# Optimization experiments

Measured on AMD Instinct MI355X. Metric: run time of the kernel, lower is better.

The kernel has to match this reference:

```python
import jax, jax.numpy as jnp
import numpy as np

BINS = 64

def _histc_rows(flat, bins):
    # flat: [N, L]; per-row torch.histc semantics with min=max=0 (use data min/max)
    lo = flat.min(axis=1, keepdims=True)
    hi = flat.max(axis=1, keepdims=True)
    same = hi == lo
    lo = jnp.where(same, lo - 1.0, lo)
    hi = jnp.where(same, hi + 1.0, hi)
    # bin index; value == hi maps to bins -> clipped into last bin (torch includes max)
    idx = jnp.floor((flat - lo) / (hi - lo) * bins).astype(jnp.int32)
    idx = jnp.clip(idx, 0, bins - 1)
    n = flat.shape[0]
    flat_idx = idx + (jnp.arange(n, dtype=jnp.int32)[:, None] * bins)
    hist = jnp.zeros((n * bins,), dtype=flat.dtype).at[flat_idx.ravel()].add(1.0)
    return hist.reshape(n, bins)

def reference(x, conv_w, conv_b, head_w, head_b):
    # Conv2d(1 -> C, k=3, valid), NCHW
    y = jax.lax.conv_general_dilated(
        x, conv_w, window_strides=(1, 1), padding='VALID',
        dimension_numbers=('NCHW', 'OIHW', 'NCHW'))
    y = y + conv_b[None, :, None, None]
    y = jax.nn.relu(y)
    b, c, h, w = y.shape
    hist = _histc_rows(y.reshape(b * c, h * w), BINS)  # [B*C, bins]
    feat = hist.reshape(b, c * BINS)
    return feat @ head_w.T + head_b

def setup_inputs() -> dict:
    key = jax.random.key(0)
    k1, k2, k3, k4, k5 = jax.random.split(key, 5)
    C, K, F = 64, 3, 1000
    return {
        'x': jax.random.normal(k1, (64, 1, 256, 256), dtype=jnp.float32),
        'conv_w': jax.random.normal(k2, (C, 1, K, K), dtype=jnp.float32) * 0.1,
        'conv_b': jax.random.normal(k3, (C,), dtype=jnp.float32) * 0.1,
        'head_w': jax.random.normal(k4, (F, C * BINS), dtype=jnp.float32) * 0.02,
        'head_b': jax.random.normal(k5, (F,), dtype=jnp.float32) * 0.02,
    }
```

## Files before the change

kernel.cpp:

```cpp
#include <hip/hip_runtime.h>


typedef short bf16x8 __attribute__((ext_vector_type(8)));
typedef float f32x16 __attribute__((ext_vector_type(16)));
typedef float f32x2 __attribute__((ext_vector_type(2)));

#define TPITCH 35
#define F_OUT_ 1000
#define KDIM_ 4096

__device__ __forceinline__ unsigned f2bf(float f) {
    unsigned u = __float_as_uint(f);
    return (u + 0x7FFFu + ((u >> 16) & 1u)) >> 16;
}
__device__ __forceinline__ float bf2f(unsigned h) { return __uint_as_float(h << 16); }

__device__ __forceinline__ unsigned cvt_u32_sat(float f) {
    unsigned r;
    asm volatile("v_cvt_u32_f32 %0, %1" : "=v"(r) : "v"(f));
    return r;
}

union FragU { uint4 u; bf16x8 v; };

__global__ __launch_bounds__(512, 6) void conv_minmax_kernel(
    const float* __restrict__ x, const float* __restrict__ cw,
    const float* __restrict__ cb, float* __restrict__ featQ,
    float* __restrict__ mnbuf, float* __restrict__ mxbuf)
{
    __shared__ unsigned t32[256 * TPITCH];
    __shared__ float red[1024];

    const int tid = threadIdx.x;
    const int lane = tid & 63;
    const int w = __builtin_amdgcn_readfirstlane(tid >> 6);
    const int b = blockIdx.x;
    const int seg = blockIdx.y;
    const int mrow = lane & 31;
    const int kg = lane >> 5;
    const int r0 = seg * 32;
    const int vlim = min(32, 254 - r0);

    featQ[(seg * 64 + b) * 512 + tid] = 0.f;

    FragU bwh[2], bwl[2];
#pragma unroll
    for (int g = 0; g < 2; ++g) {
        int och = g * 32 + mrow;
        unsigned hh[8], ll[8];
#pragma unroll
        for (int j = 0; j < 8; ++j) {
            int k = kg * 8 + j, dr = k >> 2, dc = k & 3;
            float wv = (kg == 1 && j == 7) ? cb[och]
                     : ((dr < 3 && dc < 3) ? cw[och * 9 + dr * 3 + dc] : 0.f);
            unsigned h = f2bf(wv);
            hh[j] = h;
            ll[j] = f2bf(wv - bf2f(h));
        }
        bwh[g].u = make_uint4(hh[0] | (hh[1] << 16), hh[2] | (hh[3] << 16),
                              hh[4] | (hh[5] << 16), hh[6] | (hh[7] << 16));
        bwl[g].u = make_uint4(ll[0] | (ll[1] << 16), ll[2] | (ll[3] << 16),
                              ll[4] | (ll[5] << 16), ll[6] | (ll[7] << 16));
    }
    f32x16 zc;
#pragma unroll
    for (int r = 0; r < 16; ++r) zc[r] = 0.f;

    const float* xb = x + (size_t)b * 65536;
    for (int i = tid; i < TPITCH * 256; i += 512) {
        int lrow = i >> 8, col = i & 255;
        int grow = r0 + lrow;
        float v = (grow < 256) ? xb[grow * 256 + col] : 0.f;
        unsigned h = f2bf(v);
        unsigned l = f2bf(v - bf2f(h));
        t32[col * TPITCH + lrow] = (l << 16) | h;
    }
    __syncthreads();

    f32x2 mn2A = {3.4e38f, 3.4e38f}, mx2A = {-3.4e38f, -3.4e38f};
    f32x2 mn2B = {3.4e38f, 3.4e38f}, mx2B = {-3.4e38f, -3.4e38f};
    const int cbase = w * 32;
    const int cend = min(cbase + 32, 254);
    const unsigned* tb = t32 + mrow + 2 * kg;
    unsigned a0 = tb[cbase * TPITCH],       r1a = tb[cbase * TPITCH + 1];
    unsigned a1 = tb[(cbase + 1) * TPITCH], r1b = tb[(cbase + 1) * TPITCH + 1];
#pragma unroll 2
    for (int c = cbase; c < cend; ++c) {
        unsigned a2 = tb[(c + 2) * TPITCH];
        unsigned r1c = tb[(c + 2) * TPITCH + 1];
        FragU ah, al;
        ah.u = make_uint4(__builtin_amdgcn_perm(a1, a0, 0x05040100u), a2,
                          __builtin_amdgcn_perm(r1b, r1a, 0x05040100u),
                          (r1c & 0xFFFFu) | 0x3F800000u);
        al.u = make_uint4(__builtin_amdgcn_perm(a1, a0, 0x07060302u), a2 >> 16,
                          __builtin_amdgcn_perm(r1b, r1a, 0x07060302u), r1c >> 16);
        a0 = a1; a1 = a2; r1a = r1b; r1b = r1c;
        f32x16 accA = __builtin_amdgcn_mfma_f32_32x32x16_bf16(ah.v, bwh[0].v, zc, 0, 0, 0);
        f32x16 accB = __builtin_amdgcn_mfma_f32_32x32x16_bf16(ah.v, bwh[1].v, zc, 0, 0, 0);
        accA = __builtin_amdgcn_mfma_f32_32x32x16_bf16(al.v, bwh[0].v, accA, 0, 0, 0);
        accB = __builtin_amdgcn_mfma_f32_32x32x16_bf16(al.v, bwh[1].v, accB, 0, 0, 0);
        accA = __builtin_amdgcn_mfma_f32_32x32x16_bf16(ah.v, bwl[0].v, accA, 0, 0, 0);
        accB = __builtin_amdgcn_mfma_f32_32x32x16_bf16(ah.v, bwl[1].v, accB, 0, 0, 0);
        if (vlim >= 32) {
#pragma unroll
            for (int r = 0; r < 16; r += 2) {
                f32x2 vA = {accA[r], accA[r + 1]}, vB = {accB[r], accB[r + 1]};
                mn2A = __builtin_elementwise_min(mn2A, vA);
                mx2A = __builtin_elementwise_max(mx2A, vA);
                mn2B = __builtin_elementwise_min(mn2B, vB);
                mx2B = __builtin_elementwise_max(mx2B, vB);
            }
        } else {
#pragma unroll
            for (int r = 0; r < 16; ++r) {
                int crow = (r & 3) + 8 * (r >> 2) + 4 * kg;
                float vA = (crow < vlim) ? accA[r] : accA[0];
                float vB = (crow < vlim) ? accB[r] : accB[0];
                mn2A[0] = fminf(mn2A[0], vA); mx2A[0] = fmaxf(mx2A[0], vA);
                mn2B[0] = fminf(mn2B[0], vB); mx2B[0] = fmaxf(mx2B[0], vB);
            }
        }
    }

    float mnA = fminf(mn2A[0], mn2A[1]), mxA = fmaxf(mx2A[0], mx2A[1]);
    float mnB = fminf(mn2B[0], mn2B[1]), mxB = fmaxf(mx2B[0], mx2B[1]);
    mnA = fminf(mnA, __shfl_xor(mnA, 32, 64));
    mxA = fmaxf(mxA, __shfl_xor(mxA, 32, 64));
    mnB = fminf(mnB, __shfl_xor(mnB, 32, 64));
    mxB = fmaxf(mxB, __shfl_xor(mxB, 32, 64));
    __syncthreads();
    if (lane < 32) {
        red[w * 64 + mrow] = mnA;        red[512 + w * 64 + mrow] = mxA;
        red[w * 64 + 32 + mrow] = mnB;   red[512 + w * 64 + 32 + mrow] = mxB;
    }
    __syncthreads();
    if (tid < 64) {
        float a = red[tid], c = red[512 + tid];
#pragma unroll
        for (int i = 1; i < 8; ++i) {
            a = fminf(a, red[i * 64 + tid]);
            c = fmaxf(c, red[512 + i * 64 + tid]);
        }
        mnbuf[((b * 64 + tid) << 3) | seg] = a;
        mxbuf[((b * 64 + tid) << 3) | seg] = c;
    }
}

__global__ __launch_bounds__(512, 6) void conv_hist_kernel(
    const float* __restrict__ x, const float* __restrict__ cw,
    const float* __restrict__ cb, float* __restrict__ featQ,
    const float* __restrict__ mnbuf, const float* __restrict__ mxbuf)
{
    __shared__ unsigned t32[256 * TPITCH];
    __shared__ unsigned hist[65 * 32];

    const int tid = threadIdx.x;
    const int lane = tid & 63;
    const int w = __builtin_amdgcn_readfirstlane(tid >> 6);
    const int b = blockIdx.x;
    const int seg = blockIdx.y;
    const int gz = blockIdx.z;
    const int mrow = lane & 31;
    const int kg = lane >> 5;
    const int r0 = seg * 32;
    const int vlim = min(32, 254 - r0);
    const int och = gz * 32 + mrow;

    float rmn = 3.402823466e38f, rmx = -3.402823466e38f;
#pragma unroll
    for (int s = 0; s < 8; ++s) {
        rmn = fminf(rmn, mnbuf[((b * 64 + och) << 3) | s]);
        rmx = fmaxf(rmx, mxbuf[((b * 64 + och) << 3) | s]);
    }
    float lo = fmaxf(rmn, 0.f);
    float hi = fmaxf(rmx, 0.f);
    if (hi == lo) { lo -= 1.f; hi += 1.f; }
    const float sc = 63.984f / (hi - lo);
    const float nls = -lo * sc;
    for (int i = tid; i < 65 * 32; i += 512) hist[i] = 0u;

    FragU bwh, bwl;
    {
        unsigned hh[8], ll[8];
#pragma unroll
        for (int j = 0; j < 8; ++j) {
            int k = kg * 8 + j, dr = k >> 2, dc = k & 3;
            float wv = (kg == 1 && j == 7) ? fmaf(cb[och], sc, nls)
                     : ((dr < 3 && dc < 3) ? cw[och * 9 + dr * 3 + dc] * sc : 0.f);
            unsigned h = f2bf(wv);
            hh[j] = h;
            ll[j] = f2bf(wv - bf2f(h));
        }
        bwh.u = make_uint4(hh[0] | (hh[1] << 16), hh[2] | (hh[3] << 16),
                           hh[4] | (hh[5] << 16), hh[6] | (hh[7] << 16));
        bwl.u = make_uint4(ll[0] | (ll[1] << 16), ll[2] | (ll[3] << 16),
                           ll[4] | (ll[5] << 16), ll[6] | (ll[7] << 16));
    }
    f32x16 zc;
#pragma unroll
    for (int r = 0; r < 16; ++r) zc[r] = 0.f;

    const float* xb = x + (size_t)b * 65536;
    for (int i = tid; i < TPITCH * 256; i += 512) {
        int lrow = i >> 8, col = i & 255;
        int grow = r0 + lrow;
        float v = (grow < 256) ? xb[grow * 256 + col] : 0.f;
        unsigned h = f2bf(v);
        unsigned l = f2bf(v - bf2f(h));
        t32[col * TPITCH + lrow] = (l << 16) | h;
    }
    __syncthreads();

    const int cbase = w * 32;
    const int cend = min(cbase + 32, 254);
    unsigned* hrow = hist + mrow;
    const unsigned* tb = t32 + mrow + 2 * kg;
    unsigned a0 = tb[cbase * TPITCH],       r1a = tb[cbase * TPITCH + 1];
    unsigned a1 = tb[(cbase + 1) * TPITCH], r1b = tb[(cbase + 1) * TPITCH + 1];
#pragma unroll 2
    for (int c = cbase; c < cend; ++c) {
        unsigned a2 = tb[(c + 2) * TPITCH];
        unsigned r1c = tb[(c + 2) * TPITCH + 1];
        FragU ah, al;
        ah.u = make_uint4(__builtin_amdgcn_perm(a1, a0, 0x05040100u), a2,
                          __builtin_amdgcn_perm(r1b, r1a, 0x05040100u),
                          (r1c & 0xFFFFu) | 0x3F800000u);
        al.u = make_uint4(__builtin_amdgcn_perm(a1, a0, 0x07060302u), a2 >> 16,
                          __builtin_amdgcn_perm(r1b, r1a, 0x07060302u), r1c >> 16);
        a0 = a1; a1 = a2; r1a = r1b; r1b = r1c;
        f32x16 acc = __builtin_amdgcn_mfma_f32_32x32x16_bf16(ah.v, bwh.v, zc, 0, 0, 0);
        acc = __builtin_amdgcn_mfma_f32_32x32x16_bf16(al.v, bwh.v, acc, 0, 0, 0);
        acc = __builtin_amdgcn_mfma_f32_32x32x16_bf16(ah.v, bwl.v, acc, 0, 0, 0);
        if (vlim >= 32) {
#pragma unroll
            for (int r = 0; r < 16; ++r) {
                unsigned bin = cvt_u32_sat(acc[r]);
                atomicAdd(&hrow[bin << 5], 1u);
            }
        } else {
#pragma unroll
            for (int r = 0; r < 16; ++r) {
                int crow = (r & 3) + 8 * (r >> 2) + 4 * kg;
                unsigned bin = cvt_u32_sat(acc[r]);
                if (crow >= vlim) bin = 64u;
                atomicAdd(&hrow[bin << 5], 1u);
            }
        }
    }
    __syncthreads();

    for (int i = tid; i < 2048; i += 512) {
        int o = i >> 6, bin = i & 63;
        float cnt = (float)hist[(bin << 5) + o];
        int k = ((gz * 32 + o) << 6) | bin;
        atomicAdd(&featQ[((k >> 2) << 8) | (b << 2) | (k & 3)], cnt);
    }
}

__global__ __launch_bounds__(512) void head_kernel(
    const float* __restrict__ featQ, const float* __restrict__ hw,
    float* __restrict__ part)
{
    __shared__ float red[8][8][64];
    const int tid = threadIdx.x;
    const int m = tid & 63;
    const int kh = __builtin_amdgcn_readfirstlane(tid >> 6);
    const int n0 = blockIdx.x * 8;
    const int q = blockIdx.y;
    const int kqbase = q * 256 + kh * 32;
    const float* fb = featQ + kqbase * 256 + (m << 2);
    const float* wp[8];
#pragma unroll
    for (int c = 0; c < 8; ++c)
        wp[c] = hw + (size_t)(n0 + c) * KDIM_ + (kqbase << 2);

    float a[8] = {0.f, 0.f, 0.f, 0.f, 0.f, 0.f, 0.f, 0.f};
#pragma unroll 2
    for (int kq = 0; kq < 32; ++kq) {
        float4 f = *(const float4*)(fb + (kq << 8));
#pragma unroll
        for (int c = 0; c < 8; ++c) {
            float4 u = *(const float4*)(wp[c] + (kq << 2));
            a[c] += f.x * u.x + f.y * u.y + f.z * u.z + f.w * u.w;
        }
    }
#pragma unroll
    for (int c = 0; c < 8; ++c) red[kh][c][m] = a[c];
    __syncthreads();
    {
        int c = tid >> 6, mm = tid & 63;
        float v = 0.f;
#pragma unroll
        for (int j = 0; j < 8; ++j) v += red[j][c][mm];
        part[(size_t)q * 64000 + (n0 + c) * 64 + mm] = v;
    }
}

__global__ __launch_bounds__(256) void head_reduce_kernel(
    const float* __restrict__ part, const float* __restrict__ hb,
    float* __restrict__ out)
{
    int idx = blockIdx.x * 256 + threadIdx.x;
    int n = idx >> 6, m = idx & 63;
    float v = hb[n] + part[idx] + part[64000 + idx] +
              part[128000 + idx] + part[192000 + idx];
    out[(size_t)m * F_OUT_ + n] = v;
}

extern "C" void kernel_launch(void* const* d_in, const int* in_sizes, int n_in,
                              void* d_out, int out_size, void* d_ws, size_t ws_size,
                              hipStream_t stream) {
    const float* x      = (const float*)d_in[0];
    const float* conv_w = (const float*)d_in[1];
    const float* conv_b = (const float*)d_in[2];
    const float* head_w = (const float*)d_in[3];
    const float* head_b = (const float*)d_in[4];
    float* out   = (float*)d_out;
    float* featQ = (float*)d_ws;
    float* mnbuf = featQ + 262144;
    float* mxbuf = mnbuf + 32768;
    float* part  = mxbuf + 32768;

    dim3 g1(64, 8);
    dim3 g2(64, 8, 2);
    conv_minmax_kernel<<<g1, 512, 0, stream>>>(x, conv_w, conv_b, featQ, mnbuf, mxbuf);
    conv_hist_kernel<<<g2, 512, 0, stream>>>(x, conv_w, conv_b, featQ, mnbuf, mxbuf);
    head_kernel<<<dim3(125, 4), 512, 0, stream>>>(featQ, head_w, part);
    head_reduce_kernel<<<250, 256, 0, stream>>>(part, head_b, out);
}
```

Measured before the change: 186.3 us.

## Merge both channel groups into one histogram block and prefetch LDS rows ahead

The histogram kernel now handles all 64 output channels per block with two MFMA accumulator sets, instead of launching a second z-slice per 32 channels. This halves the redundant input staging and bf16 split conversion of the image tile, at the cost of more registers and a larger shared histogram. Both conv kernels also load the next input column one iteration early to hide LDS latency, and replace the paired vector min/max with scalar fminf/fmaxf chains. The occupancy hint drops from 6 to 4 blocks to allow the extra register pressure.

```diff
diff --git a/kernel.cpp b/kernel.cpp
--- a/kernel.cpp
+++ b/kernel.cpp
@@ -3,7 +3,6 @@
 
 typedef short bf16x8 __attribute__((ext_vector_type(8)));
 typedef float f32x16 __attribute__((ext_vector_type(16)));
-typedef float f32x2 __attribute__((ext_vector_type(2)));
 
 #define TPITCH 35
 #define F_OUT_ 1000
@@ -23,7 +22,7 @@
 
 union FragU { uint4 u; bf16x8 v; };
 
-__global__ __launch_bounds__(512, 6) void conv_minmax_kernel(
+__global__ __launch_bounds__(512, 4) void conv_minmax_kernel(
     const float* __restrict__ x, const float* __restrict__ cw,
     const float* __restrict__ cb, float* __restrict__ featQ,
     float* __restrict__ mnbuf, float* __restrict__ mxbuf)
@@ -77,24 +76,26 @@
     }
     __syncthreads();
 
-    f32x2 mn2A = {3.4e38f, 3.4e38f}, mx2A = {-3.4e38f, -3.4e38f};
-    f32x2 mn2B = {3.4e38f, 3.4e38f}, mx2B = {-3.4e38f, -3.4e38f};
+    float mnA = 3.4e38f, mxA = -3.4e38f;
+    float mnB = 3.4e38f, mxB = -3.4e38f;
     const int cbase = w * 32;
     const int cend = min(cbase + 32, 254);
     const unsigned* tb = t32 + mrow + 2 * kg;
     unsigned a0 = tb[cbase * TPITCH],       r1a = tb[cbase * TPITCH + 1];
     unsigned a1 = tb[(cbase + 1) * TPITCH], r1b = tb[(cbase + 1) * TPITCH + 1];
+    unsigned a2 = tb[(cbase + 2) * TPITCH], r1c = tb[(cbase + 2) * TPITCH + 1];
 #pragma unroll 2
     for (int c = cbase; c < cend; ++c) {
-        unsigned a2 = tb[(c + 2) * TPITCH];
-        unsigned r1c = tb[(c + 2) * TPITCH + 1];
+        int cp = min(c + 3, 255);
+        unsigned a3  = tb[cp * TPITCH];
+        unsigned r1d = tb[cp * TPITCH + 1];
         FragU ah, al;
         ah.u = make_uint4(__builtin_amdgcn_perm(a1, a0, 0x05040100u), a2,
                           __builtin_amdgcn_perm(r1b, r1a, 0x05040100u),
                           (r1c & 0xFFFFu) | 0x3F800000u);
         al.u = make_uint4(__builtin_amdgcn_perm(a1, a0, 0x07060302u), a2 >> 16,
                           __builtin_amdgcn_perm(r1b, r1a, 0x07060302u), r1c >> 16);
-        a0 = a1; a1 = a2; r1a = r1b; r1b = r1c;
+        a0 = a1; a1 = a2; a2 = a3; r1a = r1b; r1b = r1c; r1c = r1d;
         f32x16 accA = __builtin_amdgcn_mfma_f32_32x32x16_bf16(ah.v, bwh[0].v, zc, 0, 0, 0);
         f32x16 accB = __builtin_amdgcn_mfma_f32_32x32x16_bf16(ah.v, bwh[1].v, zc, 0, 0, 0);
         accA = __builtin_amdgcn_mfma_f32_32x32x16_bf16(al.v, bwh[0].v, accA, 0, 0, 0);
@@ -104,11 +105,10 @@
         if (vlim >= 32) {
 #pragma unroll
             for (int r = 0; r < 16; r += 2) {
-                f32x2 vA = {accA[r], accA[r + 1]}, vB = {accB[r], accB[r + 1]};
-                mn2A = __builtin_elementwise_min(mn2A, vA);
-                mx2A = __builtin_elementwise_max(mx2A, vA);
-                mn2B = __builtin_elementwise_min(mn2B, vB);
-                mx2B = __builtin_elementwise_max(mx2B, vB);
+                mnA = fminf(fminf(mnA, accA[r]), accA[r + 1]);
+                mxA = fmaxf(fmaxf(mxA, accA[r]), accA[r + 1]);
+                mnB = fminf(fminf(mnB, accB[r]), accB[r + 1]);
+                mxB = fmaxf(fmaxf(mxB, accB[r]), accB[r + 1]);
             }
         } else {
 #pragma unroll
@@ -116,14 +116,12 @@
                 int crow = (r & 3) + 8 * (r >> 2) + 4 * kg;
                 float vA = (crow < vlim) ? accA[r] : accA[0];
                 float vB = (crow < vlim) ? accB[r] : accB[0];
-                mn2A[0] = fminf(mn2A[0], vA); mx2A[0] = fmaxf(mx2A[0], vA);
-                mn2B[0] = fminf(mn2B[0], vB); mx2B[0] = fmaxf(mx2B[0], vB);
+                mnA = fminf(mnA, vA); mxA = fmaxf(mxA, vA);
+                mnB = fminf(mnB, vB); mxB = fmaxf(mxB, vB);
             }
         }
     }
 
-    float mnA = fminf(mn2A[0], mn2A[1]), mxA = fmaxf(mx2A[0], mx2A[1]);
-    float mnB = fminf(mn2B[0], mn2B[1]), mxB = fmaxf(mx2B[0], mx2B[1]);
     mnA = fminf(mnA, __shfl_xor(mnA, 32, 64));
     mxA = fmaxf(mxA, __shfl_xor(mxA, 32, 64));
     mnB = fminf(mnB, __shfl_xor(mnB, 32, 64));
@@ -146,41 +144,47 @@
     }
 }
 
-__global__ __launch_bounds__(512, 6) void conv_hist_kernel(
+__global__ __launch_bounds__(512, 4) void conv_hist_kernel(
     const float* __restrict__ x, const float* __restrict__ cw,
     const float* __restrict__ cb, float* __restrict__ featQ,
     const float* __restrict__ mnbuf, const float* __restrict__ mxbuf)
 {
     __shared__ unsigned t32[256 * TPITCH];
-    __shared__ unsigned hist[65 * 32];
+    __shared__ unsigned hist[65 * 64];
 
     const int tid = threadIdx.x;
     const int lane = tid & 63;
     const int w = __builtin_amdgcn_readfirstlane(tid >> 6);
     const int b = blockIdx.x;
     const int seg = blockIdx.y;
-    const int gz = blockIdx.z;
     const int mrow = lane & 31;
     const int kg = lane >> 5;
     const int r0 = seg * 32;
     const int vlim = min(32, 254 - r0);
-    const int och = gz * 32 + mrow;
-
-    float rmn = 3.402823466e38f, rmx = -3.402823466e38f;
-#pragma unroll
-    for (int s = 0; s < 8; ++s) {
-        rmn = fminf(rmn, mnbuf[((b * 64 + och) << 3) | s]);
-        rmx = fmaxf(rmx, mxbuf[((b * 64 + och) << 3) | s]);
-    }
-    float lo = fmaxf(rmn, 0.f);
-    float hi = fmaxf(rmx, 0.f);
-    if (hi == lo) { lo -= 1.f; hi += 1.f; }
-    const float sc = 63.984f / (hi - lo);
-    const float nls = -lo * sc;
-    for (int i = tid; i < 65 * 32; i += 512) hist[i] = 0u;
-
-    FragU bwh, bwl;
-    {
+
+    float scS[2], nlsS[2];
+#pragma unroll
+    for (int g = 0; g < 2; ++g) {
+        int och = g * 32 + mrow;
+        float rmn = 3.402823466e38f, rmx = -3.402823466e38f;
+#pragma unroll
+        for (int s = 0; s < 8; ++s) {
+            rmn = fminf(rmn, mnbuf[((b * 64 + och) << 3) | s]);
+            rmx = fmaxf(rmx, mxbuf[((b * 64 + och) << 3) | s]);
+        }
+        float lo = fmaxf(rmn, 0.f);
+        float hi = fmaxf(rmx, 0.f);
+        if (hi == lo) { lo -= 1.f; hi += 1.f; }
+        scS[g] = 63.984f / (hi - lo);
+        nlsS[g] = -lo * scS[g];
+    }
+    for (int i = tid; i < 65 * 64; i += 512) hist[i] = 0u;
+
+    FragU bwh[2], bwl[2];
+#pragma unroll
+    for (int g = 0; g < 2; ++g) {
+        int och = g * 32 + mrow;
+        float sc = scS[g], nls = nlsS[g];
         unsigned hh[8], ll[8];
 #pragma unroll
         for (int j = 0; j < 8; ++j) {
@@ -191,10 +195,10 @@
             hh[j] = h;
             ll[j] = f2bf(wv - bf2f(h));
         }
-        bwh.u = make_uint4(hh[0] | (hh[1] << 16), hh[2] | (hh[3] << 16),
-                           hh[4] | (hh[5] << 16), hh[6] | (hh[7] << 16));
-        bwl.u = make_uint4(ll[0] | (ll[1] << 16), ll[2] | (ll[3] << 16),
-                           ll[4] | (ll[5] << 16), ll[6] | (ll[7] << 16));
+        bwh[g].u = make_uint4(hh[0] | (hh[1] << 16), hh[2] | (hh[3] << 16),
+                              hh[4] | (hh[5] << 16), hh[6] | (hh[7] << 16));
+        bwl[g].u = make_uint4(ll[0] | (ll[1] << 16), ll[2] | (ll[3] << 16),
+                              ll[4] | (ll[5] << 16), ll[6] | (ll[7] << 16));
     }
     f32x16 zc;
 #pragma unroll
@@ -217,42 +221,51 @@
     const unsigned* tb = t32 + mrow + 2 * kg;
     unsigned a0 = tb[cbase * TPITCH],       r1a = tb[cbase * TPITCH + 1];
     unsigned a1 = tb[(cbase + 1) * TPITCH], r1b = tb[(cbase + 1) * TPITCH + 1];
+    unsigned a2 = tb[(cbase + 2) * TPITCH], r1c = tb[(cbase + 2) * TPITCH + 1];
 #pragma unroll 2
     for (int c = cbase; c < cend; ++c) {
-        unsigned a2 = tb[(c + 2) * TPITCH];
-        unsigned r1c = tb[(c + 2) * TPITCH + 1];
+        int cp = min(c + 3, 255);
+        unsigned a3  = tb[cp * TPITCH];
+        unsigned r1d = tb[cp * TPITCH + 1];
         FragU ah, al;
         ah.u = make_uint4(__builtin_amdgcn_perm(a1, a0, 0x05040100u), a2,
                           __builtin_amdgcn_perm(r1b, r1a, 0x05040100u),
                           (r1c & 0xFFFFu) | 0x3F800000u);
         al.u = make_uint4(__builtin_amdgcn_perm(a1, a0, 0x07060302u), a2 >> 16,
                           __builtin_amdgcn_perm(r1b, r1a, 0x07060302u), r1c >> 16);
-        a0 = a1; a1 = a2; r1a = r1b; r1b = r1c;
-        f32x16 acc = __builtin_amdgcn_mfma_f32_32x32x16_bf16(ah.v, bwh.v, zc, 0, 0, 0);
-        acc = __builtin_amdgcn_mfma_f32_32x32x16_bf16(al.v, bwh.v, acc, 0, 0, 0);
-        acc = __builtin_amdgcn_mfma_f32_32x32x16_bf16(ah.v, bwl.v, acc, 0, 0, 0);
+        a0 = a1; a1 = a2; a2 = a3; r1a = r1b; r1b = r1c; r1c = r1d;
+        f32x16 accA = __builtin_amdgcn_mfma_f32_32x32x16_bf16(ah.v, bwh[0].v, zc, 0, 0, 0);
+        f32x16 accB = __builtin_amdgcn_mfma_f32_32x32x16_bf16(ah.v, bwh[1].v, zc, 0, 0, 0);
+        accA = __builtin_amdgcn_mfma_f32_32x32x16_bf16(al.v, bwh[0].v, accA, 0, 0, 0);
+        accB = __builtin_amdgcn_mfma_f32_32x32x16_bf16(al.v, bwh[1].v, accB, 0, 0, 0);
+        accA = __builtin_amdgcn_mfma_f32_32x32x16_bf16(ah.v, bwl[0].v, accA, 0, 0, 0);
+        accB = __builtin_amdgcn_mfma_f32_32x32x16_bf16(ah.v, bwl[1].v, accB, 0, 0, 0);
         if (vlim >= 32) {
 #pragma unroll
             for (int r = 0; r < 16; ++r) {
-                unsigned bin = cvt_u32_sat(acc[r]);
-                atomicAdd(&hrow[bin << 5], 1u);
+                unsigned binA = cvt_u32_sat(accA[r]);
+                unsigned binB = cvt_u32_sat(accB[r]);
+                atomicAdd(&hrow[binA << 6], 1u);
+                atomicAdd(&hrow[(binB << 6) + 32], 1u);
             }
         } else {
 #pragma unroll
             for (int r = 0; r < 16; ++r) {
                 int crow = (r & 3) + 8 * (r >> 2) + 4 * kg;
-                unsigned bin = cvt_u32_sat(acc[r]);
-                if (crow >= vlim) bin = 64u;
-                atomicAdd(&hrow[bin << 5], 1u);
+                unsigned binA = cvt_u32_sat(accA[r]);
+                unsigned binB = cvt_u32_sat(accB[r]);
+                if (crow >= vlim) { binA = 64u; binB = 64u; }
+                atomicAdd(&hrow[binA << 6], 1u);
+                atomicAdd(&hrow[(binB << 6) + 32], 1u);
             }
         }
     }
     __syncthreads();
 
-    for (int i = tid; i < 2048; i += 512) {
+    for (int i = tid; i < 4096; i += 512) {
         int o = i >> 6, bin = i & 63;
-        float cnt = (float)hist[(bin << 5) + o];
-        int k = ((gz * 32 + o) << 6) | bin;
+        float cnt = (float)hist[(bin << 6) + o];
+        int k = (o << 6) | bin;
         atomicAdd(&featQ[((k >> 2) << 8) | (b << 2) | (k & 3)], cnt);
     }
 }
@@ -322,7 +335,7 @@
     float* part  = mxbuf + 32768;
 
     dim3 g1(64, 8);
-    dim3 g2(64, 8, 2);
+    dim3 g2(64, 8);
     conv_minmax_kernel<<<g1, 512, 0, stream>>>(x, conv_w, conv_b, featQ, mnbuf, mxbuf);
     conv_hist_kernel<<<g2, 512, 0, stream>>>(x, conv_w, conv_b, featQ, mnbuf, mxbuf);
     head_kernel<<<dim3(125, 4), 512, 0, stream>>>(featQ, head_w, part);
```

Measured after the change: 187.4 us. Within noise of the previous version (+0.6%).

## Skip bin-zero atomics, infer bin 0 by subtraction, replace global float atomics

Applied to the files above, without the earlier changes.

The histogram kernel no longer issues LDS atomics for bin 0, which after ReLU gets most samples. Bin 0 is instead recovered in a new fixup kernel as the total pixel count (254*254) minus the sum of the other bins. Per-block histograms are packed as 16-bit pairs into a workspace buffer and reduced across row segments by the fixup kernel, replacing global float atomicAdds and the featQ zeroing. The conv loops also prefetch one column further ahead, and the min/max reduction uses scalar fminf chains. This adds a kernel launch and relies on per-block counts fitting in 16 bits.

```diff
diff --git a/kernel.cpp b/kernel.cpp
--- a/kernel.cpp
+++ b/kernel.cpp
@@ -3,7 +3,6 @@
 
 typedef short bf16x8 __attribute__((ext_vector_type(8)));
 typedef float f32x16 __attribute__((ext_vector_type(16)));
-typedef float f32x2 __attribute__((ext_vector_type(2)));
 
 #define TPITCH 35
 #define F_OUT_ 1000
@@ -25,7 +24,7 @@
 
 __global__ __launch_bounds__(512, 6) void conv_minmax_kernel(
     const float* __restrict__ x, const float* __restrict__ cw,
-    const float* __restrict__ cb, float* __restrict__ featQ,
+    const float* __restrict__ cb,
     float* __restrict__ mnbuf, float* __restrict__ mxbuf)
 {
     __shared__ unsigned t32[256 * TPITCH];
@@ -41,8 +40,6 @@
     const int r0 = seg * 32;
     const int vlim = min(32, 254 - r0);
 
-    featQ[(seg * 64 + b) * 512 + tid] = 0.f;
-
     FragU bwh[2], bwl[2];
 #pragma unroll
     for (int g = 0; g < 2; ++g) {
@@ -77,24 +74,26 @@
     }
     __syncthreads();
 
-    f32x2 mn2A = {3.4e38f, 3.4e38f}, mx2A = {-3.4e38f, -3.4e38f};
-    f32x2 mn2B = {3.4e38f, 3.4e38f}, mx2B = {-3.4e38f, -3.4e38f};
+    float mnA = 3.4e38f, mxA = -3.4e38f;
+    float mnB = 3.4e38f, mxB = -3.4e38f;
     const int cbase = w * 32;
     const int cend = min(cbase + 32, 254);
     const unsigned* tb = t32 + mrow + 2 * kg;
     unsigned a0 = tb[cbase * TPITCH],       r1a = tb[cbase * TPITCH + 1];
     unsigned a1 = tb[(cbase + 1) * TPITCH], r1b = tb[(cbase + 1) * TPITCH + 1];
+    unsigned a2 = tb[(cbase + 2) * TPITCH], r1c = tb[(cbase + 2) * TPITCH + 1];
 #pragma unroll 2
     for (int c = cbase; c < cend; ++c) {
-        unsigned a2 = tb[(c + 2) * TPITCH];
-        unsigned r1c = tb[(c + 2) * TPITCH + 1];
+        int cp = min(c + 3, 255);
+        unsigned a3  = tb[cp * TPITCH];
+        unsigned r1d = tb[cp * TPITCH + 1];
         FragU ah, al;
         ah.u = make_uint4(__builtin_amdgcn_perm(a1, a0, 0x05040100u), a2,
                           __builtin_amdgcn_perm(r1b, r1a, 0x05040100u),
                           (r1c & 0xFFFFu) | 0x3F800000u);
         al.u = make_uint4(__builtin_amdgcn_perm(a1, a0, 0x07060302u), a2 >> 16,
                           __builtin_amdgcn_perm(r1b, r1a, 0x07060302u), r1c >> 16);
-        a0 = a1; a1 = a2; r1a = r1b; r1b = r1c;
+        a0 = a1; a1 = a2; a2 = a3; r1a = r1b; r1b = r1c; r1c = r1d;
         f32x16 accA = __builtin_amdgcn_mfma_f32_32x32x16_bf16(ah.v, bwh[0].v, zc, 0, 0, 0);
         f32x16 accB = __builtin_amdgcn_mfma_f32_32x32x16_bf16(ah.v, bwh[1].v, zc, 0, 0, 0);
         accA = __builtin_amdgcn_mfma_f32_32x32x16_bf16(al.v, bwh[0].v, accA, 0, 0, 0);
@@ -104,11 +103,10 @@
         if (vlim >= 32) {
 #pragma unroll
             for (int r = 0; r < 16; r += 2) {
-                f32x2 vA = {accA[r], accA[r + 1]}, vB = {accB[r], accB[r + 1]};
-                mn2A = __builtin_elementwise_min(mn2A, vA);
-                mx2A = __builtin_elementwise_max(mx2A, vA);
-                mn2B = __builtin_elementwise_min(mn2B, vB);
-                mx2B = __builtin_elementwise_max(mx2B, vB);
+                mnA = fminf(fminf(mnA, accA[r]), accA[r + 1]);
+                mxA = fmaxf(fmaxf(mxA, accA[r]), accA[r + 1]);
+                mnB = fminf(fminf(mnB, accB[r]), accB[r + 1]);
+                mxB = fmaxf(fmaxf(mxB, accB[r]), accB[r + 1]);
             }
         } else {
 #pragma unroll
@@ -116,14 +114,12 @@
                 int crow = (r & 3) + 8 * (r >> 2) + 4 * kg;
                 float vA = (crow < vlim) ? accA[r] : accA[0];
                 float vB = (crow < vlim) ? accB[r] : accB[0];
-                mn2A[0] = fminf(mn2A[0], vA); mx2A[0] = fmaxf(mx2A[0], vA);
-                mn2B[0] = fminf(mn2B[0], vB); mx2B[0] = fmaxf(mx2B[0], vB);
+                mnA = fminf(mnA, vA); mxA = fmaxf(mxA, vA);
+                mnB = fminf(mnB, vB); mxB = fmaxf(mxB, vB);
             }
         }
     }
 
-    float mnA = fminf(mn2A[0], mn2A[1]), mxA = fmaxf(mx2A[0], mx2A[1]);
-    float mnB = fminf(mn2B[0], mn2B[1]), mxB = fmaxf(mx2B[0], mx2B[1]);
     mnA = fminf(mnA, __shfl_xor(mnA, 32, 64));
     mxA = fmaxf(mxA, __shfl_xor(mxA, 32, 64));
     mnB = fminf(mnB, __shfl_xor(mnB, 32, 64));
@@ -148,11 +144,11 @@
 
 __global__ __launch_bounds__(512, 6) void conv_hist_kernel(
     const float* __restrict__ x, const float* __restrict__ cw,
-    const float* __restrict__ cb, float* __restrict__ featQ,
+    const float* __restrict__ cb, unsigned* __restrict__ Pw,
     const float* __restrict__ mnbuf, const float* __restrict__ mxbuf)
 {
     __shared__ unsigned t32[256 * TPITCH];
-    __shared__ unsigned hist[65 * 32];
+    __shared__ unsigned hist[64 * 32];
 
     const int tid = threadIdx.x;
     const int lane = tid & 63;
@@ -177,7 +173,7 @@
     if (hi == lo) { lo -= 1.f; hi += 1.f; }
     const float sc = 63.984f / (hi - lo);
     const float nls = -lo * sc;
-    for (int i = tid; i < 65 * 32; i += 512) hist[i] = 0u;
+    for (int i = tid; i < 64 * 32; i += 512) hist[i] = 0u;
 
     FragU bwh, bwl;
     {
@@ -217,17 +213,19 @@
     const unsigned* tb = t32 + mrow + 2 * kg;
     unsigned a0 = tb[cbase * TPITCH],       r1a = tb[cbase * TPITCH + 1];
     unsigned a1 = tb[(cbase + 1) * TPITCH], r1b = tb[(cbase + 1) * TPITCH + 1];
+    unsigned a2 = tb[(cbase + 2) * TPITCH], r1c = tb[(cbase + 2) * TPITCH + 1];
 #pragma unroll 2
     for (int c = cbase; c < cend; ++c) {
-        unsigned a2 = tb[(c + 2) * TPITCH];
-        unsigned r1c = tb[(c + 2) * TPITCH + 1];
+        int cp = min(c + 3, 255);
+        unsigned a3  = tb[cp * TPITCH];
+        unsigned r1d = tb[cp * TPITCH + 1];
         FragU ah, al;
         ah.u = make_uint4(__builtin_amdgcn_perm(a1, a0, 0x05040100u), a2,
                           __builtin_amdgcn_perm(r1b, r1a, 0x05040100u),
                           (r1c & 0xFFFFu) | 0x3F800000u);
         al.u = make_uint4(__builtin_amdgcn_perm(a1, a0, 0x07060302u), a2 >> 16,
                           __builtin_amdgcn_perm(r1b, r1a, 0x07060302u), r1c >> 16);
-        a0 = a1; a1 = a2; r1a = r1b; r1b = r1c;
+        a0 = a1; a1 = a2; a2 = a3; r1a = r1b; r1b = r1c; r1c = r1d;
         f32x16 acc = __builtin_amdgcn_mfma_f32_32x32x16_bf16(ah.v, bwh.v, zc, 0, 0, 0);
         acc = __builtin_amdgcn_mfma_f32_32x32x16_bf16(al.v, bwh.v, acc, 0, 0, 0);
         acc = __builtin_amdgcn_mfma_f32_32x32x16_bf16(ah.v, bwl.v, acc, 0, 0, 0);
@@ -235,25 +233,60 @@
 #pragma unroll
             for (int r = 0; r < 16; ++r) {
                 unsigned bin = cvt_u32_sat(acc[r]);
-                atomicAdd(&hrow[bin << 5], 1u);
+                if (bin) atomicAdd(&hrow[bin << 5], 1u);
             }
         } else {
 #pragma unroll
             for (int r = 0; r < 16; ++r) {
                 int crow = (r & 3) + 8 * (r >> 2) + 4 * kg;
                 unsigned bin = cvt_u32_sat(acc[r]);
-                if (crow >= vlim) bin = 64u;
-                atomicAdd(&hrow[bin << 5], 1u);
+                if (crow >= vlim) bin = 0u;
+                if (bin) atomicAdd(&hrow[bin << 5], 1u);
             }
         }
     }
     __syncthreads();
 
-    for (int i = tid; i < 2048; i += 512) {
-        int o = i >> 6, bin = i & 63;
-        float cnt = (float)hist[(bin << 5) + o];
-        int k = ((gz * 32 + o) << 6) | bin;
-        atomicAdd(&featQ[((k >> 2) << 8) | (b << 2) | (k & 3)], cnt);
+    {
+        unsigned base = (unsigned)(seg * 128 + b * 2 + gz) * 1024u;
+        for (int j = tid; j < 1024; j += 512) {
+            uint2 hv = *(const uint2*)&hist[2 * j];
+            Pw[base + j] = (hv.y << 16) | (hv.x & 0xFFFFu);
+        }
+    }
+}
+
+__global__ __launch_bounds__(512) void hist_fixup_kernel(
+    const unsigned* __restrict__ Pw, float* __restrict__ featQ)
+{
+    const int bk = blockIdx.x;
+    const int b = bk >> 1, gz = bk & 1;
+    const int t = threadIdx.x;
+    const int bin = t & 63;
+    const int o5i = t >> 6;
+    const int half = o5i & 1;
+    unsigned s[4];
+#pragma unroll
+    for (int m = 0; m < 4; ++m) {
+        int op = (o5i >> 1) + (m << 2);
+        unsigned acc = 0;
+#pragma unroll
+        for (int seg = 0; seg < 8; ++seg)
+            acc += Pw[(unsigned)(seg * 128 + bk) * 1024u + (bin << 4) + op];
+        s[m] = half ? (acc >> 16) : (acc & 0xFFFFu);
+    }
+#pragma unroll
+    for (int m = 0; m < 4; ++m) {
+        unsigned v = (bin == 0) ? 0u : s[m];
+#pragma unroll
+        for (int d = 1; d < 64; d <<= 1) v += __shfl_xor(v, d, 64);
+        if (bin == 0) s[m] = 64516u - v;
+    }
+#pragma unroll
+    for (int m = 0; m < 4; ++m) {
+        int och5 = o5i + (m << 3);
+        int k = (((gz << 5) + och5) << 6) | bin;
+        featQ[((k >> 2) << 8) | (b << 2) | (k & 3)] = (float)s[m];
     }
 }
 
@@ -320,11 +353,13 @@
     float* mnbuf = featQ + 262144;
     float* mxbuf = mnbuf + 32768;
     float* part  = mxbuf + 32768;
+    unsigned* Pw = (unsigned*)(part + 256000);
 
     dim3 g1(64, 8);
     dim3 g2(64, 8, 2);
-    conv_minmax_kernel<<<g1, 512, 0, stream>>>(x, conv_w, conv_b, featQ, mnbuf, mxbuf);
-    conv_hist_kernel<<<g2, 512, 0, stream>>>(x, conv_w, conv_b, featQ, mnbuf, mxbuf);
+    conv_minmax_kernel<<<g1, 512, 0, stream>>>(x, conv_w, conv_b, mnbuf, mxbuf);
+    conv_hist_kernel<<<g2, 512, 0, stream>>>(x, conv_w, conv_b, Pw, mnbuf, mxbuf);
+    hist_fixup_kernel<<<128, 512, 0, stream>>>(Pw, featQ);
     head_kernel<<<dim3(125, 4), 512, 0, stream>>>(featQ, head_w, part);
     head_reduce_kernel<<<250, 256, 0, stream>>>(part, head_b, out);
 }
```

After: 192.2 us. 3.2% more time.
